# Performance work log

Measured on AMD Instinct MI355X. Metric: run time of the kernel, lower is better.

The kernel has to match this reference:

```python
import jax, jax.numpy as jnp
import numpy as np

DIM = 1024
N_HEADS = 16
HEAD_DIM = DIM // N_HEADS
HIDDEN = 4096  # round_up(4*DIM, 256)
ROPE_THETA = 10000.0
EPS = 1e-6


def setup_inputs() -> dict:
    key = jax.random.key(0)
    ks = jax.random.split(key, 10)
    s = 0.02
    return {
        "x": jax.random.normal(ks[0], (1, 4096, DIM), dtype=jnp.float32),
        "wq": jax.random.normal(ks[1], (DIM, DIM), dtype=jnp.float32) * s,
        "wk": jax.random.normal(ks[2], (DIM, DIM), dtype=jnp.float32) * s,
        "wv": jax.random.normal(ks[3], (DIM, DIM), dtype=jnp.float32) * s,
        "wo": jax.random.normal(ks[4], (DIM, DIM), dtype=jnp.float32) * s,
        "w1": jax.random.normal(ks[5], (HIDDEN, DIM), dtype=jnp.float32) * s,
        "w2": jax.random.normal(ks[6], (DIM, HIDDEN), dtype=jnp.float32) * s,
        "w3": jax.random.normal(ks[7], (HIDDEN, DIM), dtype=jnp.float32) * s,
        "g_attn": jnp.ones((DIM,), dtype=jnp.float32),
        "g_ffn": jnp.ones((DIM,), dtype=jnp.float32),
    }


def _rmsnorm(x, g):
    return x * jax.lax.rsqrt(jnp.mean(x * x, axis=-1, keepdims=True) + EPS) * g


def _rope_tables(seqlen):
    inv = 1.0 / (ROPE_THETA ** (jnp.arange(0, HEAD_DIM, 2, dtype=jnp.float32) / HEAD_DIM))
    ang = jnp.arange(seqlen, dtype=jnp.float32)[:, None] * inv[None, :]  # [s, hd/2]
    return jnp.cos(ang), jnp.sin(ang)


def _apply_rope(q, cos, sin):
    # q: [b, s, h, hd]; pairs (even, odd) treated as complex (re, im)
    b, s, h, d = q.shape
    qr = q.reshape(b, s, h, d // 2, 2)
    re, im = qr[..., 0], qr[..., 1]
    c = cos[None, :, None, :]
    sn = sin[None, :, None, :]
    out = jnp.stack([re * c - im * sn, re * sn + im * c], axis=-1)
    return out.reshape(b, s, h, d)


def reference(x, wq, wk, wv, wo, w1, w2, w3, g_attn, g_ffn):
    b, s, _ = x.shape
    xn = _rmsnorm(x, g_attn)
    q = (xn @ wq.T).reshape(b, s, N_HEADS, HEAD_DIM)
    k = (xn @ wk.T).reshape(b, s, N_HEADS, HEAD_DIM)
    v = (xn @ wv.T).reshape(b, s, N_HEADS, HEAD_DIM)
    cos, sin = _rope_tables(s)
    q = _apply_rope(q, cos, sin)
    k = _apply_rope(k, cos, sin)
    scores = jnp.einsum("bthd,bThd->bhtT", q, k) / np.sqrt(HEAD_DIM).astype(np.float32)
    probs = jax.nn.softmax(scores, axis=-1)
    attn = jnp.einsum("bhtT,bThd->bthd", probs, v).reshape(b, s, DIM)
    h = x + attn @ wo.T
    hn = _rmsnorm(h, g_ffn)
    ff = (jax.nn.silu(hn @ w1.T) * (hn @ w3.T)) @ w2.T
    return h + ff
```

## Files before the change

### kernel.cpp

```cpp
#include <hip/hip_runtime.h>

#define S_LEN 4096
#define DIMM  1024
#define NH    16
#define HD    64
#define HID   4096

typedef unsigned short u16;
typedef __attribute__((ext_vector_type(8))) short bf16x8;
typedef __attribute__((ext_vector_type(4))) short short4b;
typedef __attribute__((ext_vector_type(8))) unsigned short u16x8;
typedef __attribute__((ext_vector_type(4))) float f32x4;

__device__ __forceinline__ u16 f2bf(float f) {
  unsigned u = __float_as_uint(f);
  u += 0x7fffu + ((u >> 16) & 1u);
  return (u16)(u >> 16);
}
__device__ __forceinline__ float bf2f(u16 h) {
  return __uint_as_float(((unsigned)h) << 16);
}
__device__ __forceinline__ unsigned pack_bf16(float hi, float lo) {
  return __builtin_amdgcn_perm(__float_as_uint(hi), __float_as_uint(lo), 0x07060302u);
}
__device__ __forceinline__ float fexp2(float x) { return __builtin_amdgcn_exp2f(x); }

__device__ __forceinline__ void gl_lds16(const void* g, void* l) {
  __builtin_amdgcn_global_load_lds(
      (const __attribute__((address_space(1))) void*)g,
      (__attribute__((address_space(3))) void*)l, 16, 0, 0);
}

__global__ __launch_bounds__(256) void prep_kernel(
    const float* __restrict__ wq, const float* __restrict__ wk, const float* __restrict__ wv,
    const float* __restrict__ wo, const float* __restrict__ w1, const float* __restrict__ w3,
    const float* __restrict__ w2, const float* __restrict__ x, const float* __restrict__ g_attn,
    u16* __restrict__ wqkvb, u16* __restrict__ wob,
    u16* __restrict__ w13b, u16* __restrict__ w2b, u16* __restrict__ xnb,
    float* __restrict__ cosT, float* __restrict__ sinT) {
  int b = blockIdx.x;
  int t = threadIdx.x;
  if (b < 8192) {
    const float* src;
    u16* dst;
    size_t o;
    int i;
    if (b < 2048) {
      int which = b >> 9, lb = b & 511;
      src = which == 0 ? wq : which == 1 ? wk : which == 2 ? wv : wo;
      dst = which == 3 ? wob : wqkvb + ((size_t)which << 20);
      i = (lb * 256 + t) * 8;
      o = (size_t)i;
    } else {
      int b2 = b - 2048, which = b2 >> 11, lb = b2 & 2047;
      src = which == 0 ? w1 : which == 1 ? w3 : w2;
      i = (lb * 256 + t) * 8;
      if (which == 2) {
        dst = w2b;
        o = (size_t)i;
      } else {
        dst = w13b;
        o = ((size_t)(i & ~1023) << 1) + ((size_t)which << 10) + (i & 1023);
      }
    }
    float4 a = *(const float4*)(src + i);
    float4 c = *(const float4*)(src + i + 4);
    u16x8 r;
    r[0] = f2bf(a.x); r[1] = f2bf(a.y); r[2] = f2bf(a.z); r[3] = f2bf(a.w);
    r[4] = f2bf(c.x); r[5] = f2bf(c.y); r[6] = f2bf(c.z); r[7] = f2bf(c.w);
    *(u16x8*)(dst + o) = r;
  } else if (b < 8704) {
    int idx = (b - 8192) * 256 + t;
    int pos = idx >> 5, i = idx & 31;
    double inv = pow(10000.0, -(double)(2 * i) / 64.0);
    double a = (double)pos * inv;
    cosT[idx] = (float)cos(a);
    sinT[idx] = (float)sin(a);
  } else {
    int row = b - 8704;
    const float4 v = *(const float4*)(x + (size_t)row * DIMM + t * 4);
    float ss = v.x * v.x + v.y * v.y + v.z * v.z + v.w * v.w;
#pragma unroll
    for (int off = 32; off > 0; off >>= 1) ss += __shfl_down(ss, off);
    __shared__ float red[4];
    if ((t & 63) == 0) red[t >> 6] = ss;
    __syncthreads();
    float tot = red[0] + red[1] + red[2] + red[3];
    float sc = rsqrtf(tot * (1.0f / DIMM) + 1e-6f);
    const float4 gv = *(const float4*)(g_attn + t * 4);
    ushort4 o2;
    o2.x = f2bf(v.x * sc * gv.x);
    o2.y = f2bf(v.y * sc * gv.y);
    o2.z = f2bf(v.z * sc * gv.z);
    o2.w = f2bf(v.w * sc * gv.w);
    *(ushort4*)(xnb + (size_t)row * DIMM + t * 4) = o2;
  }
}

__global__ __launch_bounds__(256) void rmsnorm_kernel(const float* __restrict__ x, const float* __restrict__ g,
                                                      u16* __restrict__ out) {
  int row = blockIdx.x;
  int t = threadIdx.x;
  const float4 v = *(const float4*)(x + (size_t)row * DIMM + t * 4);
  float ss = v.x * v.x + v.y * v.y + v.z * v.z + v.w * v.w;
#pragma unroll
  for (int off = 32; off > 0; off >>= 1) ss += __shfl_down(ss, off);
  __shared__ float red[4];
  if ((t & 63) == 0) red[t >> 6] = ss;
  __syncthreads();
  float tot = red[0] + red[1] + red[2] + red[3];
  float sc = rsqrtf(tot * (1.0f / DIMM) + 1e-6f);
  const float4 gv = *(const float4*)(g + t * 4);
  ushort4 o;
  o.x = f2bf(v.x * sc * gv.x);
  o.y = f2bf(v.y * sc * gv.y);
  o.z = f2bf(v.z * sc * gv.z);
  o.w = f2bf(v.w * sc * gv.w);
  *(ushort4*)(out + (size_t)row * DIMM + t * 4) = o;
}

template <int OUTMODE>
__global__ __launch_bounds__(512) void gemm_kernel(const u16* __restrict__ A, const u16* __restrict__ B,
                                                   void* Cout, const float* res, int N, int K, int lda,
                                                   int ldb, const float* cosT, const float* sinT) {
  __shared__ uint4 As0[1024], Bs0[1024], As1[1024], Bs1[1024];
  const int t = threadIdx.x;
  const int w = t >> 6, l = t & 63;
  const int wm = w >> 1, wn = w & 1;
  const int bm = blockIdx.y, bn = blockIdx.x;
  const int quad = l >> 4, lc = l & 15;

  f32x4 acc[2][4];
  const f32x4 zero = {0.0f, 0.0f, 0.0f, 0.0f};
#pragma unroll
  for (int mi = 0; mi < 2; mi++)
#pragma unroll
    for (int ni = 0; ni < 4; ni++) acc[mi][ni] = zero;

  const int band0 = t >> 6, kq0 = (t >> 4) & 3, row0 = t & 15;
  const u16* Ap0 = A + (size_t)(bm * 128 + band0 * 16 + row0) * lda + kq0 * 8;
  const u16* Bp0 = B + (size_t)(bn * 128 + band0 * 16 + row0) * ldb + kq0 * 8;
  if constexpr (OUTMODE == 4) {
    Ap0 += (size_t)blockIdx.z * K;
    Bp0 += (size_t)blockIdx.z * K;
  }
  const int abase = wm * 128 + l;
  const int bbase = wn * 256 + l;

#define STAGEL(AD, BD, K0)                 \
  do {                                     \
    gl_lds16(Ap0 + (K0), &(AD)[t]);        \
    gl_lds16(Ap0 + (K0) + 32, &(AD)[t + 512]); \
    gl_lds16(Bp0 + (K0), &(BD)[t]);        \
    gl_lds16(Bp0 + (K0) + 32, &(BD)[t + 512]); \
  } while (0)

#define COMPL(AS, BS)                                                                               \
  do {                                                                                              \
    _Pragma("unroll") for (int ks = 0; ks < 2; ks++) {                                              \
      bf16x8 af[2], bfr[4];                                                                         \
      _Pragma("unroll") for (int mi = 0; mi < 2; mi++)                                              \
          af[mi] = *(const bf16x8*)&(AS)[ks * 512 + abase + mi * 64];                               \
      _Pragma("unroll") for (int ni = 0; ni < 4; ni++)                                              \
          bfr[ni] = *(const bf16x8*)&(BS)[ks * 512 + bbase + ni * 64];                              \
      _Pragma("unroll") for (int mi = 0; mi < 2; mi++)                                              \
          _Pragma("unroll") for (int ni = 0; ni < 4; ni++)                                          \
              acc[mi][ni] = __builtin_amdgcn_mfma_f32_16x16x32_bf16(af[mi], bfr[ni], acc[mi][ni], 0, 0, 0); \
    }                                                                                               \
  } while (0)

  STAGEL(As0, Bs0, 0);
  __syncthreads();
  int k0 = 0;
  for (; k0 + 128 < K; k0 += 128) {
    STAGEL(As1, Bs1, k0 + 64);
    COMPL(As0, Bs0);
    __syncthreads();
    STAGEL(As0, Bs0, k0 + 128);
    COMPL(As1, Bs1);
    __syncthreads();
  }
  STAGEL(As1, Bs1, k0 + 64);
  COMPL(As0, Bs0);
  __syncthreads();
  COMPL(As1, Bs1);
#undef STAGEL
#undef COMPL

  const int rbase = bm * 128 + wm * 32 + quad * 4;
  const int cbase = bn * 128 + wn * 64 + lc;
  const float qs = (OUTMODE == 3 && bn < 8) ? 0.18033688011112f : 1.0f;
#pragma unroll
  for (int mi = 0; mi < 2; mi++) {
#pragma unroll
    for (int r = 0; r < 4; r++) {
      int row = rbase + mi * 16 + r;
#pragma unroll
      for (int ni = 0; ni < 4; ni++) {
        int col = cbase + ni * 16;
        if constexpr (OUTMODE == 0) {
          ((u16*)Cout)[(size_t)row * N + col] = f2bf(acc[mi][ni][r]);
        } else if constexpr (OUTMODE == 1) {
          size_t idx = (size_t)row * N + col;
          ((float*)Cout)[idx] = res[idx] + acc[mi][ni][r];
        } else if constexpr (OUTMODE == 4) {
          size_t idx = (size_t)row * N + col;
          atomicAdd((float*)Cout + idx, acc[mi][ni][r]);
        } else {
          if (bn >= 16) {
            int vcol = col - 2048, key = row;
            int h = vcol >> 6, din = vcol & 63, kb = key >> 6, k63 = key & 63;
            int off = ((h << 6) + kb) * 4096 + (((din >> 4) << 1) + (k63 >> 5)) * 512 +
                      ((((k63 >> 2) & 3) << 4) + (din & 15)) * 8 + ((k63 >> 4) & 1) * 4 + (k63 & 3);
            ((u16*)const_cast<float*>(res))[off] = f2bf(acc[mi][ni][r]);
          } else {
            float v = acc[mi][ni][r];
            float pv = __shfl_xor(v, 1);
            int i = ((ni * 16 + lc) & 63) >> 1;
            float c = cosT[(row << 5) + i], s = sinT[(row << 5) + i];
            float o = (lc & 1) ? (pv * s + v * c) : (v * c - pv * s);
            ((u16*)Cout)[(size_t)row * N + col] = f2bf(o * qs);
          }
        }
      }
    }
  }
}

__global__ __launch_bounds__(512) void gemm256_kernel(const u16* __restrict__ A, const u16* __restrict__ B,
                                                      u16* __restrict__ Cout, int N, int K, int lda) {
  __shared__ uint4 As0[1024], Bs0[1024], As1[1024], Bs1[1024], As2[1024], Bs2[1024];
  const int t = threadIdx.x;
  const int w = t >> 6, l = t & 63;
  const int wm = w >> 2, wn = w & 3;
  const int bm = blockIdx.y, bn = blockIdx.x;
  const int quad = l >> 4, lc = l & 15;

  f32x4 acc[8][4];
  const f32x4 zero = {0.0f, 0.0f, 0.0f, 0.0f};
#pragma unroll
  for (int mi = 0; mi < 8; mi++)
#pragma unroll
    for (int ni = 0; ni < 4; ni++) acc[mi][ni] = zero;

  const int band0 = t >> 6, kq0 = (t >> 4) & 3, row0 = t & 15;
  const u16* Ap0 = A + (size_t)(bm * 256 + band0 * 16 + row0) * lda + kq0 * 8;
  const u16* Bp0 = B + (size_t)(bn * 256 + band0 * 16 + row0) * K + kq0 * 8;
  const size_t Astep = (size_t)128 * lda;
  const size_t Bstep = (size_t)128 * K;

#define STG(AD, BD, K0)                           \
  do {                                            \
    gl_lds16(Ap0 + (K0), &(AD)[t]);               \
    gl_lds16(Ap0 + Astep + (K0), &(AD)[t + 512]); \
    gl_lds16(Bp0 + (K0), &(BD)[t]);               \
    gl_lds16(Bp0 + Bstep + (K0), &(BD)[t + 512]); \
  } while (0)

  const int NT = K >> 5;

#define PHASE(CA, CB, SA, SB, TT)                                              \
  do {                                                                         \
    if ((TT) + 2 < NT) STG(SA, SB, ((TT) + 2) * 32);                           \
    bf16x8 af[8], bfr[4];                                                      \
    _Pragma("unroll") for (int mi = 0; mi < 8; mi++)                           \
        af[mi] = *(const bf16x8*)&(CA)[(wm * 8 + mi) * 64 + l];                \
    _Pragma("unroll") for (int ni = 0; ni < 4; ni++)                           \
        bfr[ni] = *(const bf16x8*)&(CB)[(wn * 4 + ni) * 64 + l];               \
    __builtin_amdgcn_s_setprio(1);                                             \
    _Pragma("unroll") for (int mi = 0; mi < 8; mi++)                           \
        _Pragma("unroll") for (int ni = 0; ni < 4; ni++)                       \
            acc[mi][ni] = __builtin_amdgcn_mfma_f32_16x16x32_bf16(af[mi], bfr[ni], acc[mi][ni], 0, 0, 0); \
    __builtin_amdgcn_s_setprio(0);                                             \
    if ((TT) + 1 < NT) {                                                       \
      asm volatile("s_waitcnt lgkmcnt(0)" ::: "memory");                       \
      if ((TT) + 2 < NT) {                                                     \
        asm volatile("s_waitcnt vmcnt(4)" ::: "memory");                       \
      } else {                                                                 \
        asm volatile("s_waitcnt vmcnt(0)" ::: "memory");                       \
      }                                                                        \
      __builtin_amdgcn_s_barrier();                                            \
    }                                                                          \
  } while (0)

  STG(As0, Bs0, 0);
  STG(As1, Bs1, 32);
  asm volatile("s_waitcnt vmcnt(4)" ::: "memory");
  __builtin_amdgcn_s_barrier();

  for (int tt = 0; tt < NT; tt += 3) {
    PHASE(As0, Bs0, As2, Bs2, tt);
    if (tt + 1 < NT) PHASE(As1, Bs1, As0, Bs0, tt + 1);
    if (tt + 2 < NT) PHASE(As2, Bs2, As1, Bs1, tt + 2);
  }
#undef STG
#undef PHASE

  const int rbase = bm * 256 + wm * 128 + quad * 4;
  const int cbase = bn * 256 + wn * 64 + lc;
  const int ffw = N >> 1;
  const bool isu = (l & 1) == 0;
  const float nl2e = -1.44269504088896f;
#pragma unroll
  for (int mi = 0; mi < 8; mi++) {
#pragma unroll
    for (int r = 0; r < 4; r++) {
      int row = rbase + mi * 16 + r;
#pragma unroll
      for (int ni = 0; ni < 4; ni++) {
        int col = cbase + ni * 16;
        float v = acc[mi][ni][r];
        float pv = __shfl_xor(v, 1);
        if (isu) {
          float sig = __builtin_amdgcn_rcpf(1.0f + fexp2(v * nl2e));
          Cout[(size_t)row * ffw + (col >> 1)] = f2bf(v * sig * pv);
        }
      }
    }
  }
}

__global__ __launch_bounds__(512) void attn_kernel(const u16* __restrict__ Qm, const u16* __restrict__ Km,
                                                   const u16* __restrict__ Vsw, u16* __restrict__ Om) {
  __shared__ char smem[32768];
  uint4* Ks0 = (uint4*)smem;
  uint4* Vs0 = (uint4*)(smem + 8192);
  uint4* Ks1 = (uint4*)(smem + 16384);
  uint4* Vs1 = (uint4*)(smem + 24576);
  const int t = threadIdx.x;
  const int w = t >> 6, l = t & 63;
  const int quad = l >> 4, lc = l & 15;
  const int hd = blockIdx.y;
  const int qrow = blockIdx.x * 128 + w * 16;

  bf16x8 qf_[2];
#pragma unroll
  for (int ch = 0; ch < 2; ch++)
    qf_[ch] = *(const bf16x8*)(Qm + (size_t)(qrow + lc) * 2048 + hd * HD + ch * 32 + quad * 8);

  const f32x4 zero = {0.0f, 0.0f, 0.0f, 0.0f};
  const bf16x8 ones8 = {(short)0x3F80, (short)0x3F80, (short)0x3F80, (short)0x3F80,
                        (short)0x3F80, (short)0x3F80, (short)0x3F80, (short)0x3F80};
  f32x4 Oa[4];
#pragma unroll
  for (int df = 0; df < 4; df++) Oa[df] = zero;
  f32x4 lsacc = zero;

  const int s0 = t >> 7, c0 = (t >> 6) & 1, kq0 = (t >> 4) & 3, row0 = t & 15;
  const u16* Kp0 = Km + (size_t)(s0 * 16 + row0) * 2048 + hd * HD + c0 * 32 + kq0 * 8;
  const u16* Vp = Vsw + (size_t)(hd * HD) * 4096 + t * 8;

#define STAGEKV(KD, VD, TT)                                  \
  do {                                                       \
    gl_lds16(Kp0 + (size_t)(TT)*131072, &(KD)[t]);           \
    gl_lds16(Vp + (size_t)(TT)*4096, &(VD)[t]);              \
  } while (0)

#define TILE_COMPUTE(KS, VS)                                                                 \
  do {                                                                                       \
    f32x4 Sf[4];                                                                             \
    _Pragma("unroll") for (int kf = 0; kf < 4; kf++) {                                       \
      bf16x8 ka = *(const bf16x8*)&(KS)[kf * 128 + l];                                       \
      bf16x8 kb2 = *(const bf16x8*)&(KS)[kf * 128 + 64 + l];                                 \
      f32x4 z = __builtin_amdgcn_mfma_f32_16x16x32_bf16(ka, qf_[0], zero, 0, 0, 0);          \
      z = __builtin_amdgcn_mfma_f32_16x16x32_bf16(kb2, qf_[1], z, 0, 0, 0);                  \
      Sf[kf] = z;                                                                            \
    }                                                                                        \
    _Pragma("unroll") for (int kf = 0; kf < 4; kf++)                                         \
        _Pragma("unroll") for (int r = 0; r < 4; r++)                                        \
      Sf[kf][r] = fexp2(Sf[kf][r]);                                                          \
    union { bf16x8 v8; uint2 u2[2]; } p0, p1;                                                \
    p0.u2[0].x = pack_bf16(Sf[0][1], Sf[0][0]);                                              \
    p0.u2[0].y = pack_bf16(Sf[0][3], Sf[0][2]);                                              \
    p0.u2[1].x = pack_bf16(Sf[1][1], Sf[1][0]);                                              \
    p0.u2[1].y = pack_bf16(Sf[1][3], Sf[1][2]);                                              \
    p1.u2[0].x = pack_bf16(Sf[2][1], Sf[2][0]);                                              \
    p1.u2[0].y = pack_bf16(Sf[2][3], Sf[2][2]);                                              \
    p1.u2[1].x = pack_bf16(Sf[3][1], Sf[3][0]);                                              \
    p1.u2[1].y = pack_bf16(Sf[3][3], Sf[3][2]);                                              \
    lsacc = __builtin_amdgcn_mfma_f32_16x16x32_bf16(ones8, p0.v8, lsacc, 0, 0, 0);           \
    lsacc = __builtin_amdgcn_mfma_f32_16x16x32_bf16(ones8, p1.v8, lsacc, 0, 0, 0);           \
    _Pragma("unroll") for (int df = 0; df < 4; df++) {                                       \
      bf16x8 va = *(const bf16x8*)&(VS)[(df * 2) * 64 + l];                                  \
      bf16x8 vb = *(const bf16x8*)&(VS)[(df * 2 + 1) * 64 + l];                              \
      Oa[df] = __builtin_amdgcn_mfma_f32_16x16x32_bf16(va, p0.v8, Oa[df], 0, 0, 0);          \
      Oa[df] = __builtin_amdgcn_mfma_f32_16x16x32_bf16(vb, p1.v8, Oa[df], 0, 0, 0);          \
    }                                                                                        \
  } while (0)

  STAGEKV(Ks0, Vs0, 0);
  __syncthreads();

  for (int tt = 0; tt < 64; tt += 2) {
    STAGEKV(Ks1, Vs1, tt + 1);
    TILE_COMPUTE(Ks0, Vs0);
    __syncthreads();
    if (tt + 2 < 64) STAGEKV(Ks0, Vs0, tt + 2);
    TILE_COMPUTE(Ks1, Vs1);
    __syncthreads();
  }
#undef STAGEKV
#undef TILE_COMPUTE

  u16* ep = (u16*)smem;
  float invl = 1.0f / lsacc[0];
#pragma unroll
  for (int df = 0; df < 4; df++) {
    int qb = w * 16 + lc;
    int d = df * 16 + quad * 4;
    uint2 pv;
    pv.x = pack_bf16(Oa[df][1] * invl, Oa[df][0] * invl);
    pv.y = pack_bf16(Oa[df][3] * invl, Oa[df][2] * invl);
    *(uint2*)(ep + qb * 72 + d) = pv;
  }
  __syncthreads();
#pragma unroll
  for (int it = 0; it < 2; it++) {
    int qb = it * 64 + (t >> 3);
    int dp = (t & 7) * 8;
    u16x8 rowv = *(const u16x8*)(ep + qb * 72 + dp);
    *(u16x8*)(Om + (size_t)(blockIdx.x * 128 + qb) * DIMM + hd * HD + dp) = rowv;
  }
}

extern "C" void kernel_launch(void* const* d_in, const int* in_sizes, int n_in,
                              void* d_out, int out_size, void* d_ws, size_t ws_size,
                              hipStream_t stream) {
  const float* x      = (const float*)d_in[0];
  const float* wq     = (const float*)d_in[1];
  const float* wk     = (const float*)d_in[2];
  const float* wv     = (const float*)d_in[3];
  const float* wo     = (const float*)d_in[4];
  const float* w1     = (const float*)d_in[5];
  const float* w2     = (const float*)d_in[6];
  const float* w3     = (const float*)d_in[7];
  const float* g_attn = (const float*)d_in[8];
  const float* g_ffn  = (const float*)d_in[9];
  float* out = (float*)d_out;
  char* ws = (char*)d_ws;
  const size_t MB = 1ull << 20;

  u16* wqkvb = (u16*)(ws + 0 * MB);
  u16* wob  = (u16*)(ws + 6 * MB);
  u16* w13b = (u16*)(ws + 8 * MB);
  u16* w2b  = (u16*)(ws + 24 * MB);
  u16* xnb  = (u16*)(ws + 32 * MB);
  u16* qkb  = (u16*)(ws + 40 * MB);
  u16* vswz = (u16*)(ws + 56 * MB);
  u16* attb = (u16*)(ws + 64 * MB);
  u16* ff   = (u16*)(ws + 40 * MB);
  float* cosT = (float*)(ws + 104 * MB);
  float* sinT = (float*)(ws + 104 * MB + 512 * 1024);

  prep_kernel<<<12800, 256, 0, stream>>>(wq, wk, wv, wo, w1, w3, w2, x, g_attn,
                                         wqkvb, wob, w13b, w2b, xnb, cosT, sinT);

  gemm_kernel<3><<<dim3(24, 32), 512, 0, stream>>>(xnb, wqkvb, qkb, (const float*)vswz,
                                                   2048, DIMM, DIMM, DIMM, cosT, sinT);

  attn_kernel<<<dim3(32, 16), 512, 0, stream>>>(qkb, qkb + 1024, vswz, attb);

  gemm_kernel<1><<<dim3(8, 32), 512, 0, stream>>>(attb, wob, out, x, DIMM, DIMM, DIMM, DIMM, nullptr, nullptr);

  rmsnorm_kernel<<<4096, 256, 0, stream>>>(out, g_ffn, xnb);

  gemm256_kernel<<<dim3(32, 16), 512, 0, stream>>>(xnb, w13b, ff, 8192, DIMM, DIMM);

  gemm_kernel<4><<<dim3(8, 32, 2), 512, 0, stream>>>(ff, w2b, out, nullptr, DIMM, 2048, 4096, HID, nullptr, nullptr);
}
```

Before: 471.8 us.

## Deepen gemm256 pipeline to four LDS stages with register double-buffering

The 256x256 GEMM moves from a three-stage to a four-stage LDS ring, so global-to-LDS copies are issued three tiles ahead. It also double-buffers the MFMA operand fragments in registers: the next tile's LDS reads overlap the current tile's MFMAs. The aim is to hide LDS read latency and global load latency behind matrix math. In exchange, LDS use rises to 128 KB and operand register use doubles. The added `launch_bounds(512, 2)` could push the compiler into register caps or spills with 128 accumulator floats per thread.

```diff
diff --git a/kernel.cpp b/kernel.cpp
--- a/kernel.cpp
+++ b/kernel.cpp
@@ -227,9 +227,10 @@
   }
 }
 
-__global__ __launch_bounds__(512) void gemm256_kernel(const u16* __restrict__ A, const u16* __restrict__ B,
-                                                      u16* __restrict__ Cout, int N, int K, int lda) {
-  __shared__ uint4 As0[1024], Bs0[1024], As1[1024], Bs1[1024], As2[1024], Bs2[1024];
+__global__ __launch_bounds__(512, 2) void gemm256_kernel(const u16* __restrict__ A, const u16* __restrict__ B,
+                                                         u16* __restrict__ Cout, int N, int K, int lda) {
+  __shared__ uint4 As0[1024], Bs0[1024], As1[1024], Bs1[1024],
+                   As2[1024], Bs2[1024], As3[1024], Bs3[1024];
   const int t = threadIdx.x;
   const int w = t >> 6, l = t & 63;
   const int wm = w >> 2, wn = w & 3;
@@ -257,24 +258,35 @@
     gl_lds16(Bp0 + Bstep + (K0), &(BD)[t + 512]); \
   } while (0)
 
+#define RDREG(AF, BF, AS, BS)                                                  \
+  do {                                                                         \
+    _Pragma("unroll") for (int mi = 0; mi < 8; mi++)                           \
+        AF[mi] = *(const bf16x8*)&(AS)[(wm * 8 + mi) * 64 + l];                \
+    _Pragma("unroll") for (int ni = 0; ni < 4; ni++)                           \
+        BF[ni] = *(const bf16x8*)&(BS)[(wn * 4 + ni) * 64 + l];                \
+  } while (0)
+
+#define MMA(AF, BF)                                                                                 \
+  do {                                                                                              \
+    __builtin_amdgcn_s_setprio(1);                                                                  \
+    _Pragma("unroll") for (int mi = 0; mi < 8; mi++)                                                \
+        _Pragma("unroll") for (int ni = 0; ni < 4; ni++)                                            \
+            acc[mi][ni] = __builtin_amdgcn_mfma_f32_16x16x32_bf16(AF[mi], BF[ni], acc[mi][ni], 0, 0, 0); \
+    __builtin_amdgcn_s_setprio(0);                                                                  \
+  } while (0)
+
   const int NT = K >> 5;
 
-#define PHASE(CA, CB, SA, SB, TT)                                              \
+  bf16x8 afA[8], bfA[4], afB[8], bfB[4];
+
+#define PH(TT, CURA, CURB, NXTA, NXTB, SA, SB, RA_, RB_)                       \
   do {                                                                         \
-    if ((TT) + 2 < NT) STG(SA, SB, ((TT) + 2) * 32);                           \
-    bf16x8 af[8], bfr[4];                                                      \
-    _Pragma("unroll") for (int mi = 0; mi < 8; mi++)                           \
-        af[mi] = *(const bf16x8*)&(CA)[(wm * 8 + mi) * 64 + l];                \
-    _Pragma("unroll") for (int ni = 0; ni < 4; ni++)                           \
-        bfr[ni] = *(const bf16x8*)&(CB)[(wn * 4 + ni) * 64 + l];               \
-    __builtin_amdgcn_s_setprio(1);                                             \
-    _Pragma("unroll") for (int mi = 0; mi < 8; mi++)                           \
-        _Pragma("unroll") for (int ni = 0; ni < 4; ni++)                       \
-            acc[mi][ni] = __builtin_amdgcn_mfma_f32_16x16x32_bf16(af[mi], bfr[ni], acc[mi][ni], 0, 0, 0); \
-    __builtin_amdgcn_s_setprio(0);                                             \
+    if ((TT) + 3 < NT) STG(SA, SB, ((TT) + 3) * 32);                           \
+    if ((TT) + 1 < NT) RDREG(NXTA, NXTB, RA_, RB_);                            \
+    MMA(CURA, CURB);                                                           \
     if ((TT) + 1 < NT) {                                                       \
       asm volatile("s_waitcnt lgkmcnt(0)" ::: "memory");                       \
-      if ((TT) + 2 < NT) {                                                     \
+      if ((TT) + 3 < NT) {                                                     \
         asm volatile("s_waitcnt vmcnt(4)" ::: "memory");                       \
       } else {                                                                 \
         asm volatile("s_waitcnt vmcnt(0)" ::: "memory");                       \
@@ -285,16 +297,23 @@
 
   STG(As0, Bs0, 0);
   STG(As1, Bs1, 32);
+  STG(As2, Bs2, 64);
   asm volatile("s_waitcnt vmcnt(4)" ::: "memory");
   __builtin_amdgcn_s_barrier();
-
-  for (int tt = 0; tt < NT; tt += 3) {
-    PHASE(As0, Bs0, As2, Bs2, tt);
-    if (tt + 1 < NT) PHASE(As1, Bs1, As0, Bs0, tt + 1);
-    if (tt + 2 < NT) PHASE(As2, Bs2, As1, Bs1, tt + 2);
+  RDREG(afA, bfA, As0, Bs0);
+  asm volatile("s_waitcnt lgkmcnt(0)" ::: "memory");
+  __builtin_amdgcn_s_barrier();
+
+  for (int tt = 0; tt < NT; tt += 4) {
+    PH(tt,     afA, bfA, afB, bfB, As3, Bs3, As1, Bs1);
+    PH(tt + 1, afB, bfB, afA, bfA, As0, Bs0, As2, Bs2);
+    PH(tt + 2, afA, bfA, afB, bfB, As1, Bs1, As3, Bs3);
+    PH(tt + 3, afB, bfB, afA, bfA, As2, Bs2, As0, Bs0);
   }
 #undef STG
-#undef PHASE
+#undef RDREG
+#undef MMA
+#undef PH
 
   const int rbase = bm * 256 + wm * 128 + quad * 4;
   const int cbase = bn * 256 + wn * 64 + lc;
```

Result: slower. 490.3 us (+3.9%).
